# Optimization experiments

Measured on AMD Instinct MI355X. Metric: run time of the kernel, lower is better.

Reference implementation:

```python
import jax, jax.numpy as jnp
import numpy as np

N_NODES = 50000
N_RAND_EDGES = 800000
HEADS = 4
OUT_DIM = 64
NEG_SLOPE = 0.2  # DGL GATConv default


def _gat_layer(x, w, b, al, ar, src, dst, residual):
    """DGL-style GATConv: x [N, Fin] -> [N, H, D]."""
    n = x.shape[0]
    feat = (x @ w).reshape(n, HEADS, OUT_DIM)                # [N,H,D]
    el = jnp.sum(feat * al, axis=-1)                         # [N,H]
    er = jnp.sum(feat * ar, axis=-1)                         # [N,H]
    e = jax.nn.leaky_relu(el[src] + er[dst], NEG_SLOPE)      # [E,H]
    # segment softmax over incoming edges of each dst node
    emax = jax.ops.segment_max(e, dst, num_segments=n)       # [N,H]
    ee = jnp.exp(e - emax[dst])                              # [E,H]
    denom = jax.ops.segment_sum(ee, dst, num_segments=n)     # [N,H]
    alpha = ee / denom[dst]                                  # [E,H]
    msg = feat[src] * alpha[..., None]                       # [E,H,D]
    rst = jax.ops.segment_sum(msg, dst, num_segments=n)      # [N,H,D]
    if residual:
        rst = rst + x.reshape(n, HEADS, OUT_DIM)             # identity residual (Fin == H*D)
    return rst + b.reshape(HEADS, OUT_DIM)


def setup_inputs() -> dict:
    key = jax.random.key(0)
    ks = jax.random.split(key, 10)
    d = HEADS * OUT_DIM  # 256
    x = jax.random.normal(ks[0], (N_NODES, OUT_DIM), dtype=jnp.float32)
    w1 = jax.random.normal(ks[1], (OUT_DIM, d), dtype=jnp.float32) / np.sqrt(OUT_DIM)
    b1 = jnp.zeros((d,), dtype=jnp.float32)
    al1 = jax.random.normal(ks[2], (HEADS, OUT_DIM), dtype=jnp.float32) / np.sqrt(OUT_DIM)
    ar1 = jax.random.normal(ks[3], (HEADS, OUT_DIM), dtype=jnp.float32) / np.sqrt(OUT_DIM)
    w2 = jax.random.normal(ks[4], (d, d), dtype=jnp.float32) / np.sqrt(d)
    b2 = jnp.zeros((d,), dtype=jnp.float32)
    al2 = jax.random.normal(ks[5], (HEADS, OUT_DIM), dtype=jnp.float32) / np.sqrt(OUT_DIM)
    ar2 = jax.random.normal(ks[6], (HEADS, OUT_DIM), dtype=jnp.float32) / np.sqrt(OUT_DIM)
    loops = jnp.arange(N_NODES, dtype=jnp.int32)  # add_self_loop
    src = jnp.concatenate([jax.random.randint(ks[7], (N_RAND_EDGES,), 0, N_NODES, dtype=jnp.int32), loops])
    dst = jnp.concatenate([jax.random.randint(ks[8], (N_RAND_EDGES,), 0, N_NODES, dtype=jnp.int32), loops])
    return {"x": x, "w1": w1, "b1": b1, "al1": al1, "ar1": ar1,
            "w2": w2, "b2": b2, "al2": al2, "ar2": ar2, "src": src, "dst": dst}


def reference(x, w1, b1, al1, ar1, w2, b2, al2, ar2, src, dst):
    h = _gat_layer(x, w1, b1, al1, ar1, src, dst, residual=False)
    h = h.reshape(h.shape[0], -1)  # flatten(1) -> [N, H*D]
    h = _gat_layer(h, w2, b2, al2, ar2, src, dst, residual=True)
    return h.reshape(h.shape[0], -1)  # [N, H*D]
```

## Files before the change

kernel.cpp:

```cpp
#include <hip/hip_runtime.h>
#include <hip/hip_fp16.h>
#include <math.h>

#define HEADS 4
#define DIM 64
#define FEAT 256

__device__ inline float4 h4f(uint2 u) {
    __half2 a = __builtin_bit_cast(__half2, u.x);
    __half2 b = __builtin_bit_cast(__half2, u.y);
    float2 fa = __half22float2(a), fb = __half22float2(b);
    return make_float4(fa.x, fa.y, fb.x, fb.y);
}

__global__ __launch_bounds__(256) void hist_kernel(const int* __restrict__ dst,
                                                   int* __restrict__ deg, int E) {
    int i = blockIdx.x * blockDim.x + threadIdx.x;
    if (i < E) atomicAdd(&deg[dst[i]], 1);
}

__global__ __launch_bounds__(1024) void scan_block_kernel(const int* __restrict__ deg,
                                                          int* __restrict__ offs,
                                                          int* __restrict__ bsum, int n) {
    __shared__ int wsum[16];
    int tid = threadIdx.x, lane = tid & 63, w = tid >> 6;
    int i = blockIdx.x * 1024 + tid;
    int v = (i < n) ? deg[i] : 0;
    int x = v;
    #pragma unroll
    for (int off = 1; off < 64; off <<= 1) {
        int t = __shfl_up(x, off);
        if (lane >= off) x += t;
    }
    if (lane == 63) wsum[w] = x;
    __syncthreads();
    if (w == 0 && lane < 16) {
        int y = wsum[lane];
        #pragma unroll
        for (int off = 1; off < 16; off <<= 1) {
            int t = __shfl_up(y, off);
            if (lane >= off) y += t;
        }
        wsum[lane] = y;
    }
    __syncthreads();
    int wbase = (w == 0) ? 0 : wsum[w - 1];
    if (i < n) offs[i] = wbase + (x - v);
    if (tid == 0) bsum[blockIdx.x] = wsum[15];
}

__global__ __launch_bounds__(64) void scan_small_kernel(const int* __restrict__ bsum,
                                                        int* __restrict__ bofs, int nb) {
    int lane = threadIdx.x;
    int v = (lane < nb) ? bsum[lane] : 0;
    int x = v;
    #pragma unroll
    for (int off = 1; off < 64; off <<= 1) {
        int t = __shfl_up(x, off);
        if (lane >= off) x += t;
    }
    if (lane < nb) bofs[lane] = x - v;
    if (lane == nb - 1) bofs[nb] = x;
}

__global__ __launch_bounds__(256) void scan_add_kernel(int* __restrict__ offs,
                                                       const int* __restrict__ bofs,
                                                       int n, int nb) {
    int i = blockIdx.x * blockDim.x + threadIdx.x;
    if (i < n)       offs[i] += bofs[i >> 10];
    else if (i == n) offs[n]  = bofs[nb];
}

__global__ __launch_bounds__(256) void scatter_kernel(const int* __restrict__ src,
                                                      const int* __restrict__ dst,
                                                      const int* __restrict__ offs,
                                                      int* __restrict__ cur,
                                                      int* __restrict__ esrc, int E) {
    int i = blockIdx.x * blockDim.x + threadIdx.x;
    if (i < E) {
        int d = dst[i];
        int pos = offs[d] + atomicAdd(&cur[d], 1);
        esrc[pos] = src[i];
    }
}

#define GBM 128
#define GBN 128
#define GBK 16
__global__ __launch_bounds__(256) void gemm_f32h(const float* __restrict__ A,
                                                 const float* __restrict__ B,
                                                 __half* __restrict__ C,
                                                 int M, int Nc, int K) {
    __shared__ float As[GBK][GBM];
    __shared__ float Bs[GBK][GBN];
    int tid = threadIdx.x;
    int m0 = blockIdx.x * GBM;
    int n0 = blockIdx.y * GBN;
    int tr = tid >> 4;
    int tc = tid & 15;

    float acc[8][8];
    #pragma unroll
    for (int i = 0; i < 8; ++i)
        #pragma unroll
        for (int j = 0; j < 8; ++j) acc[i][j] = 0.f;

    for (int k0 = 0; k0 < K; k0 += GBK) {
        #pragma unroll
        for (int i = 0; i < 2; ++i) {
            int f  = tid * 2 + i;
            int r  = f >> 2;
            int c4 = (f & 3) << 2;
            int gr = m0 + r;
            float4 v = make_float4(0.f, 0.f, 0.f, 0.f);
            if (gr < M) v = *(const float4*)(A + (size_t)gr * K + k0 + c4);
            As[c4 + 0][r] = v.x; As[c4 + 1][r] = v.y;
            As[c4 + 2][r] = v.z; As[c4 + 3][r] = v.w;
        }
        #pragma unroll
        for (int i = 0; i < 2; ++i) {
            int f  = tid * 2 + i;
            int r  = f >> 5;
            int c4 = (f & 31) << 2;
            float4 v = *(const float4*)(B + (size_t)(k0 + r) * Nc + n0 + c4);
            *(float4*)(&Bs[r][c4]) = v;
        }
        __syncthreads();
        #pragma unroll
        for (int k = 0; k < GBK; ++k) {
            float ra[8], rb[8];
            *(float4*)(ra)     = *(const float4*)(&As[k][tr * 8]);
            *(float4*)(ra + 4) = *(const float4*)(&As[k][tr * 8 + 4]);
            *(float4*)(rb)     = *(const float4*)(&Bs[k][tc * 8]);
            *(float4*)(rb + 4) = *(const float4*)(&Bs[k][tc * 8 + 4]);
            #pragma unroll
            for (int i = 0; i < 8; ++i)
                #pragma unroll
                for (int j = 0; j < 8; ++j)
                    acc[i][j] = fmaf(ra[i], rb[j], acc[i][j]);
        }
        __syncthreads();
    }
    #pragma unroll
    for (int i = 0; i < 8; ++i) {
        int gr = m0 + tr * 8 + i;
        if (gr < M) {
            alignas(16) __half h[8];
            #pragma unroll
            for (int j = 0; j < 8; ++j) h[j] = __float2half_rn(acc[i][j]);
            *(uint4*)(C + (size_t)gr * Nc + n0 + tc * 8) = *(uint4*)h;
        }
    }
}

__global__ __launch_bounds__(256) void eler_kernel(const __half* __restrict__ feat,
                                                   const float* __restrict__ al,
                                                   const float* __restrict__ ar,
                                                   float* __restrict__ el,
                                                   float* __restrict__ er, int n_nodes) {
    int wid  = (blockIdx.x * blockDim.x + threadIdx.x) >> 6;
    int lane = threadIdx.x & 63;
    if (wid >= n_nodes) return;
    float4 f = h4f(*(const uint2*)(feat + (size_t)wid * FEAT + lane * 4));
    float4 a = *(const float4*)(al + lane * 4);
    float4 b = *(const float4*)(ar + lane * 4);
    float sl = f.x * a.x + f.y * a.y + f.z * a.z + f.w * a.w;
    float sr = f.x * b.x + f.y * b.y + f.z * b.z + f.w * b.w;
    #pragma unroll
    for (int off = 1; off < 16; off <<= 1) {
        sl += __shfl_xor(sl, off);
        sr += __shfl_xor(sr, off);
    }
    if ((lane & 15) == 0) {
        el[(size_t)wid * 4 + (lane >> 4)] = sl;
        er[(size_t)wid * 4 + (lane >> 4)] = sr;
    }
}

__global__ __launch_bounds__(256) void aggregate_kernel(const __half* __restrict__ feat,
                                                        const float* __restrict__ el,
                                                        const float* __restrict__ er,
                                                        const int* __restrict__ offs,
                                                        const int* __restrict__ esrc,
                                                        const float* resid,
                                                        const float* __restrict__ bias,
                                                        float* out, int n_nodes) {
    __shared__ float p_lds[4][256];
    int tid  = threadIdx.x;
    int wib  = tid >> 6;
    int lane = tid & 63;
    int n    = (blockIdx.x * blockDim.x + tid) >> 6;
    if (n >= n_nodes) return;
    int hi = lane >> 4;
    float* pw = p_lds[wib];

    int beg = offs[n], end = offs[n + 1];
    float4 er4 = *(const float4*)(er + (size_t)n * 4);

    float m0 = -1e30f, m1 = -1e30f, m2 = -1e30f, m3 = -1e30f;
    float s = 0.f;
    float4 acc = make_float4(0.f, 0.f, 0.f, 0.f);

    for (int cbeg = beg; cbeg < end; cbeg += 64) {
        int cnt = end - cbeg; if (cnt > 64) cnt = 64;
        int idx = cbeg + lane; if (idx >= end) idx = end - 1;
        int sn_l = esrc[idx];

        float4 el4 = *(const float4*)(el + (size_t)sn_l * 4);
        float e0 = el4.x + er4.x, e1 = el4.y + er4.y;
        float e2 = el4.z + er4.z, e3 = el4.w + er4.w;
        e0 = e0 >= 0.f ? e0 : 0.2f * e0;
        e1 = e1 >= 0.f ? e1 : 0.2f * e1;
        e2 = e2 >= 0.f ? e2 : 0.2f * e2;
        e3 = e3 >= 0.f ? e3 : 0.2f * e3;
        if (lane >= cnt) { e0 = e1 = e2 = e3 = -1e30f; }

        float c0 = e0, c1 = e1, c2 = e2, c3 = e3;
        #pragma unroll
        for (int off = 32; off; off >>= 1) {
            c0 = fmaxf(c0, __shfl_xor(c0, off));
            c1 = fmaxf(c1, __shfl_xor(c1, off));
            c2 = fmaxf(c2, __shfl_xor(c2, off));
            c3 = fmaxf(c3, __shfl_xor(c3, off));
        }
        float n0 = fmaxf(m0, c0), n1 = fmaxf(m1, c1);
        float n2 = fmaxf(m2, c2), n3 = fmaxf(m3, c3);
        float sc0 = __expf(m0 - n0), sc1 = __expf(m1 - n1);
        float sc2 = __expf(m2 - n2), sc3 = __expf(m3 - n3);
        float p0 = __expf(e0 - n0), p1 = __expf(e1 - n1);
        float p2 = __expf(e2 - n2), p3 = __expf(e3 - n3);
        *(float4*)(&pw[lane * 4]) = make_float4(p0, p1, p2, p3);
        asm volatile("" ::: "memory");

        float t0 = p0, t1 = p1, t2 = p2, t3 = p3;
        #pragma unroll
        for (int off = 32; off; off >>= 1) {
            t0 += __shfl_xor(t0, off);
            t1 += __shfl_xor(t1, off);
            t2 += __shfl_xor(t2, off);
            t3 += __shfl_xor(t3, off);
        }
        float sc_own = (hi & 2) ? ((hi & 1) ? sc3 : sc2) : ((hi & 1) ? sc1 : sc0);
        float t_own  = (hi & 2) ? ((hi & 1) ? t3  : t2 ) : ((hi & 1) ? t1  : t0 );
        s = s * sc_own + t_own;
        acc.x *= sc_own; acc.y *= sc_own; acc.z *= sc_own; acc.w *= sc_own;
        m0 = n0; m1 = n1; m2 = n2; m3 = n3;

        int ng = (cnt + 3) >> 2;
        uint2 fA0, fA1, fA2, fA3, fB0, fB1, fB2, fB3;

        #define LOADG(F0, F1, F2, F3, G4)                                       \
            {                                                                   \
                int j0_ = (G4);                                                 \
                int s0_ = __shfl(sn_l, j0_),     s1_ = __shfl(sn_l, j0_ + 1);   \
                int s2_ = __shfl(sn_l, j0_ + 2), s3_ = __shfl(sn_l, j0_ + 3);   \
                F0 = *(const uint2*)(feat + (size_t)s0_ * FEAT + lane * 4);     \
                F1 = *(const uint2*)(feat + (size_t)s1_ * FEAT + lane * 4);     \
                F2 = *(const uint2*)(feat + (size_t)s2_ * FEAT + lane * 4);     \
                F3 = *(const uint2*)(feat + (size_t)s3_ * FEAT + lane * 4);     \
            }
        #define COMPG(F0, F1, F2, F3, G4)                                       \
            {                                                                   \
                int j0_ = (G4);                                                 \
                float q0_ = pw[j0_ * 4 + hi],       q1_ = pw[(j0_ + 1) * 4 + hi]; \
                float q2_ = pw[(j0_ + 2) * 4 + hi], q3_ = pw[(j0_ + 3) * 4 + hi]; \
                float4 g0_ = h4f(F0), g1_ = h4f(F1), g2_ = h4f(F2), g3_ = h4f(F3); \
                acc.x += q0_ * g0_.x + q1_ * g1_.x + q2_ * g2_.x + q3_ * g3_.x; \
                acc.y += q0_ * g0_.y + q1_ * g1_.y + q2_ * g2_.y + q3_ * g3_.y; \
                acc.z += q0_ * g0_.z + q1_ * g1_.z + q2_ * g2_.z + q3_ * g3_.z; \
                acc.w += q0_ * g0_.w + q1_ * g1_.w + q2_ * g2_.w + q3_ * g3_.w; \
            }

        LOADG(fA0, fA1, fA2, fA3, 0)
        int g = 0;
        while (true) {
            if (g + 1 < ng) LOADG(fB0, fB1, fB2, fB3, (g + 1) * 4)
            COMPG(fA0, fA1, fA2, fA3, g * 4)
            ++g; if (g >= ng) break;
            if (g + 1 < ng) LOADG(fA0, fA1, fA2, fA3, (g + 1) * 4)
            COMPG(fB0, fB1, fB2, fB3, g * 4)
            ++g; if (g >= ng) break;
        }
        #undef LOADG
        #undef COMPG
    }

    float inv = 1.f / s;
    float4 r = make_float4(acc.x * inv, acc.y * inv, acc.z * inv, acc.w * inv);
    if (resid) {
        float4 rv = *(const float4*)(resid + (size_t)n * FEAT + lane * 4);
        r.x += rv.x; r.y += rv.y; r.z += rv.z; r.w += rv.w;
    }
    float4 bv = *(const float4*)(bias + lane * 4);
    r.x += bv.x; r.y += bv.y; r.z += bv.z; r.w += bv.w;
    *(float4*)(out + (size_t)n * FEAT + lane * 4) = r;
}

extern "C" void kernel_launch(void* const* d_in, const int* in_sizes, int n_in,
                              void* d_out, int out_size, void* d_ws, size_t ws_size,
                              hipStream_t stream) {
    const float* x   = (const float*)d_in[0];
    const float* w1  = (const float*)d_in[1];
    const float* b1  = (const float*)d_in[2];
    const float* al1 = (const float*)d_in[3];
    const float* ar1 = (const float*)d_in[4];
    const float* w2  = (const float*)d_in[5];
    const float* b2  = (const float*)d_in[6];
    const float* al2 = (const float*)d_in[7];
    const float* ar2 = (const float*)d_in[8];
    const int*   src = (const int*)d_in[9];
    const int*   dst = (const int*)d_in[10];
    int N = in_sizes[0] / DIM;
    int E = in_sizes[9];
    float* out = (float*)d_out;

    __half* featH = (__half*)d_ws;
    float*  el    = (float*)(featH + (size_t)N * FEAT);
    float*  er    = el + (size_t)N * 4;
    int*    deg   = (int*)(er + (size_t)N * 4);
    int*    cur   = deg + N;
    int*    offs  = cur + N;
    int*    esrc  = offs + (N + 1);
    int*    bsum  = esrc + E;
    int*    bofs  = bsum + 64;

    int nb = (N + 1023) / 1024;

    hipMemsetAsync(deg, 0, sizeof(int) * 2 * (size_t)N, stream);
    hist_kernel<<<(E + 255) / 256, 256, 0, stream>>>(dst, deg, E);
    scan_block_kernel<<<nb, 1024, 0, stream>>>(deg, offs, bsum, N);
    scan_small_kernel<<<1, 64, 0, stream>>>(bsum, bofs, nb);
    scan_add_kernel<<<(N + 256) / 256, 256, 0, stream>>>(offs, bofs, N, nb);
    scatter_kernel<<<(E + 255) / 256, 256, 0, stream>>>(src, dst, offs, cur, esrc, E);

    dim3 ggrid((N + GBM - 1) / GBM, FEAT / GBN);
    int  ngrid = (N + 3) / 4;

    gemm_f32h<<<ggrid, 256, 0, stream>>>(x, w1, featH, N, FEAT, DIM);
    eler_kernel<<<ngrid, 256, 0, stream>>>(featH, al1, ar1, el, er, N);
    aggregate_kernel<<<ngrid, 256, 0, stream>>>(featH, el, er, offs, esrc,
                                                nullptr, b1, out, N);

    gemm_f32h<<<ggrid, 256, 0, stream>>>(out, w2, featH, N, FEAT, FEAT);
    eler_kernel<<<ngrid, 256, 0, stream>>>(featH, al2, ar2, el, er, N);
    aggregate_kernel<<<ngrid, 256, 0, stream>>>(featH, el, er, offs, esrc,
                                                out, b2, out, N);
}
```

Measured before the change: 458.8 us.

## Replace FP32 SIMT GEMM with FP16 MFMA GEMM using pre-transposed weights

The scalar FP32 outer-product GEMM is replaced by a kernel that converts A tiles to fp16 in shared memory and computes with 16x16x16 f16 MFMA instructions, accumulating in fp32. A small kernel converts each weight matrix to fp16 and transposes it, so B tiles load as contiguous 16-byte rows. The aim is to use the matrix cores for the two feature projections. In exchange, inputs are rounded to fp16 before the multiply, which lowers precision, and the epilogue writes scalar halves per lane rather than vectorized rows.

```diff
diff --git a/kernel.cpp b/kernel.cpp
--- a/kernel.cpp
+++ b/kernel.cpp
@@ -5,6 +5,9 @@
 #define HEADS 4
 #define DIM 64
 #define FEAT 256
+
+typedef _Float16 half4v __attribute__((ext_vector_type(4)));
+typedef float    f32x4  __attribute__((ext_vector_type(4)));
 
 __device__ inline float4 h4f(uint2 u) {
     __half2 a = __builtin_bit_cast(__half2, u.x);
@@ -84,71 +87,102 @@
     }
 }
 
-#define GBM 128
-#define GBN 128
-#define GBK 16
-__global__ __launch_bounds__(256) void gemm_f32h(const float* __restrict__ A,
-                                                 const float* __restrict__ B,
-                                                 __half* __restrict__ C,
-                                                 int M, int Nc, int K) {
-    __shared__ float As[GBK][GBM];
-    __shared__ float Bs[GBK][GBN];
+__global__ __launch_bounds__(256) void wcvt_kernel(const float* __restrict__ w,
+                                                   __half* __restrict__ wt, int K) {
+    int id = blockIdx.x * 256 + threadIdx.x;
+    if (id < K * 256) {
+        int k = id >> 8, n = id & 255;
+        wt[n * K + k] = __float2half_rn(w[id]);
+    }
+}
+
+#define TM 128
+#define TN 128
+#define KS 32
+#define SA 40
+__global__ __launch_bounds__(256) void gemm_h(const float* __restrict__ A,
+                                              const __half* __restrict__ Bt,
+                                              __half* __restrict__ C,
+                                              int M, int K) {
+    __shared__ _Float16 As[TM * SA];
+    __shared__ _Float16 Bs[TN * SA];
     int tid = threadIdx.x;
-    int m0 = blockIdx.x * GBM;
-    int n0 = blockIdx.y * GBN;
-    int tr = tid >> 4;
-    int tc = tid & 15;
-
-    float acc[8][8];
-    #pragma unroll
-    for (int i = 0; i < 8; ++i)
-        #pragma unroll
-        for (int j = 0; j < 8; ++j) acc[i][j] = 0.f;
-
-    for (int k0 = 0; k0 < K; k0 += GBK) {
+    int wid = tid >> 6, lane = tid & 63;
+    int l15 = lane & 15, lg = lane >> 4;
+    int wr = wid >> 1, wc = wid & 1;
+    int m0 = blockIdx.x * TM;
+    int n0 = blockIdx.y * TN;
+
+    f32x4 acc[4][4];
+    #pragma unroll
+    for (int i = 0; i < 4; ++i)
+        #pragma unroll
+        for (int j = 0; j < 4; ++j) acc[i][j] = (f32x4){0.f, 0.f, 0.f, 0.f};
+
+    for (int k0 = 0; k0 < K; k0 += KS) {
         #pragma unroll
         for (int i = 0; i < 2; ++i) {
-            int f  = tid * 2 + i;
-            int r  = f >> 2;
-            int c4 = (f & 3) << 2;
-            int gr = m0 + r;
-            float4 v = make_float4(0.f, 0.f, 0.f, 0.f);
-            if (gr < M) v = *(const float4*)(A + (size_t)gr * K + k0 + c4);
-            As[c4 + 0][r] = v.x; As[c4 + 1][r] = v.y;
-            As[c4 + 2][r] = v.z; As[c4 + 3][r] = v.w;
+            int c = tid * 2 + i;
+            int row = c >> 2;
+            int kc  = (c & 3) << 3;
+            int gr  = m0 + row;
+            float4 v0 = make_float4(0.f, 0.f, 0.f, 0.f);
+            float4 v1 = make_float4(0.f, 0.f, 0.f, 0.f);
+            if (gr < M) {
+                const float* p = A + (size_t)gr * K + k0 + kc;
+                v0 = *(const float4*)p;
+                v1 = *(const float4*)(p + 4);
+            }
+            half4v h0 = {(_Float16)v0.x, (_Float16)v0.y, (_Float16)v0.z, (_Float16)v0.w};
+            half4v h1 = {(_Float16)v1.x, (_Float16)v1.y, (_Float16)v1.z, (_Float16)v1.w};
+            *(half4v*)(&As[row * SA + kc])     = h0;
+            *(half4v*)(&As[row * SA + kc + 4]) = h1;
         }
         #pragma unroll
         for (int i = 0; i < 2; ++i) {
-            int f  = tid * 2 + i;
-            int r  = f >> 5;
-            int c4 = (f & 31) << 2;
-            float4 v = *(const float4*)(B + (size_t)(k0 + r) * Nc + n0 + c4);
-            *(float4*)(&Bs[r][c4]) = v;
+            int c = tid * 2 + i;
+            int n  = c >> 2;
+            int kc = (c & 3) << 3;
+            uint4 v = *(const uint4*)(Bt + (size_t)(n0 + n) * K + k0 + kc);
+            *(uint4*)(&Bs[n * SA + kc]) = v;
         }
         __syncthreads();
-        #pragma unroll
-        for (int k = 0; k < GBK; ++k) {
-            float ra[8], rb[8];
-            *(float4*)(ra)     = *(const float4*)(&As[k][tr * 8]);
-            *(float4*)(ra + 4) = *(const float4*)(&As[k][tr * 8 + 4]);
-            *(float4*)(rb)     = *(const float4*)(&Bs[k][tc * 8]);
-            *(float4*)(rb + 4) = *(const float4*)(&Bs[k][tc * 8 + 4]);
+
+        half4v a[4][2], b[4][2];
+        #pragma unroll
+        for (int ri = 0; ri < 4; ++ri)
             #pragma unroll
-            for (int i = 0; i < 8; ++i)
+            for (int kh = 0; kh < 2; ++kh)
+                a[ri][kh] = *(const half4v*)(&As[(wr * 64 + ri * 16 + l15) * SA + kh * 16 + lg * 4]);
+        #pragma unroll
+        for (int ci = 0; ci < 4; ++ci)
+            #pragma unroll
+            for (int kh = 0; kh < 2; ++kh)
+                b[ci][kh] = *(const half4v*)(&Bs[(wc * 64 + ci * 16 + l15) * SA + kh * 16 + lg * 4]);
+
+        #pragma unroll
+        for (int kh = 0; kh < 2; ++kh)
+            #pragma unroll
+            for (int ri = 0; ri < 4; ++ri)
                 #pragma unroll
-                for (int j = 0; j < 8; ++j)
-                    acc[i][j] = fmaf(ra[i], rb[j], acc[i][j]);
-        }
+                for (int ci = 0; ci < 4; ++ci)
+                    acc[ri][ci] = __builtin_amdgcn_mfma_f32_16x16x16f16(
+                        a[ri][kh], b[ci][kh], acc[ri][ci], 0, 0, 0);
         __syncthreads();
     }
-    #pragma unroll
-    for (int i = 0; i < 8; ++i) {
-        int gr = m0 + tr * 8 + i;
-        if (gr < M) {
-            alignas(16) __half h[8];
-            #pragma unroll
-            for (int j = 0; j < 8; ++j) h[j] = __float2half_rn(acc[i][j]);
-            *(uint4*)(C + (size_t)gr * Nc + n0 + tc * 8) = *(uint4*)h;
+
+    #pragma unroll
+    for (int ri = 0; ri < 4; ++ri) {
+        #pragma unroll
+        for (int r = 0; r < 4; ++r) {
+            int grow = m0 + wr * 64 + ri * 16 + lg * 4 + r;
+            if (grow < M) {
+                #pragma unroll
+                for (int ci = 0; ci < 4; ++ci) {
+                    int gcol = n0 + wc * 64 + ci * 16 + l15;
+                    C[(size_t)grow * FEAT + gcol] = __float2half_rn(acc[ri][ci][r]);
+                }
+            }
         }
     }
 }
@@ -315,7 +349,9 @@
     float* out = (float*)d_out;
 
     __half* featH = (__half*)d_ws;
-    float*  el    = (float*)(featH + (size_t)N * FEAT);
+    __half* w1t   = featH + (size_t)N * FEAT;
+    __half* w2t   = w1t + 256 * 64;
+    float*  el    = (float*)(w2t + 256 * 256);
     float*  er    = el + (size_t)N * 4;
     int*    deg   = (int*)(er + (size_t)N * 4);
     int*    cur   = deg + N;
@@ -333,15 +369,18 @@
     scan_add_kernel<<<(N + 256) / 256, 256, 0, stream>>>(offs, bofs, N, nb);
     scatter_kernel<<<(E + 255) / 256, 256, 0, stream>>>(src, dst, offs, cur, esrc, E);
 
-    dim3 ggrid((N + GBM - 1) / GBM, FEAT / GBN);
+    wcvt_kernel<<<(64 * 256 + 255) / 256, 256, 0, stream>>>(w1, w1t, 64);
+    wcvt_kernel<<<(256 * 256 + 255) / 256, 256, 0, stream>>>(w2, w2t, 256);
+
+    dim3 ggrid((N + TM - 1) / TM, FEAT / TN);
     int  ngrid = (N + 3) / 4;
 
-    gemm_f32h<<<ggrid, 256, 0, stream>>>(x, w1, featH, N, FEAT, DIM);
+    gemm_h<<<ggrid, 256, 0, stream>>>(x, w1t, featH, N, DIM);
     eler_kernel<<<ngrid, 256, 0, stream>>>(featH, al1, ar1, el, er, N);
     aggregate_kernel<<<ngrid, 256, 0, stream>>>(featH, el, er, offs, esrc,
                                                 nullptr, b1, out, N);
 
-    gemm_f32h<<<ggrid, 256, 0, stream>>>(out, w2, featH, N, FEAT, FEAT);
+    gemm_h<<<ggrid, 256, 0, stream>>>(out, w2t, featH, N, FEAT);
     eler_kernel<<<ngrid, 256, 0, stream>>>(featH, al2, ar2, el, er, N);
     aggregate_kernel<<<ngrid, 256, 0, stream>>>(featH, el, er, offs, esrc,
                                                 out, b2, out, N);
```

New measurement: 399.0 us. -13.0%, faster.
